# Kernel tuning notes

Hardware: AMD Instinct MI355X
Metric: run time of the kernel (lower is better)

The kernel has to match this reference:

```python
import jax, jax.numpy as jnp
import numpy as np

EMB = 512        # embedding_size (asserted == 512 in ColorClassifier)
NPC = 256        # n_possible_colors (asserted == 256)


def setup_inputs() -> dict:
    key = jax.random.key(0)
    ks = jax.random.split(key, 8)
    N, D = 8192, 16
    s = 0.05  # small init scale keeps softmax/log numerically sane
    adj = jax.random.randint(ks[0], (N, D), 0, N, dtype=jnp.int32)
    W = jax.random.normal(ks[1], (EMB + NPC, EMB), jnp.float32) * s
    a = jax.random.normal(ks[2], (2 * EMB,), jnp.float32) * s
    fc1_w = jax.random.normal(ks[3], (EMB, EMB), jnp.float32) * s
    fc1_b = jnp.zeros((EMB,), jnp.float32)
    fc2_w = jax.random.normal(ks[4], (400, EMB), jnp.float32) * s
    fc2_b = jnp.zeros((400,), jnp.float32)
    fc3_w = jax.random.normal(ks[5], (NPC + 1, 400), jnp.float32) * s
    fc3_b = jnp.zeros((NPC + 1,), jnp.float32)
    return dict(adj=adj, W=W, a=a, fc1_w=fc1_w, fc1_b=fc1_b,
                fc2_w=fc2_w, fc2_b=fc2_b, fc3_w=fc3_w, fc3_b=fc3_b,
                baseline=50)


def _forward(adj, W, a, fc1_w, fc1_b, fc2_w, fc2_b, fc3_w, fc3_b, baseline):
    N, D = adj.shape
    alpha = 0.2           # GAT leaky-relu slope
    a1, a2 = a[:EMB], a[EMB:]
    NEG = -jnp.inf

    emb0 = jnp.zeros((N, EMB), jnp.float32)
    oh0 = jnp.zeros((N, NPC), jnp.float32).at[0, 0].set(1.0)   # vertex 0 gets color 0
    colors0 = jnp.full((N,), -1, jnp.int32).at[0].set(0)
    idx = jnp.arange(NPC + 1)

    def step(carry, v):
        emb, oh, colors, n_used, lpp = carry
        nbrs = adj[v]  # [D]
        # --- GAT singular attention update of vertex v (self row first) ---
        x = jnp.concatenate([
            jnp.concatenate([emb[v][None], emb[nbrs]], axis=0),
            jnp.concatenate([oh[v][None], oh[nbrs]], axis=0)], axis=1)  # [D+1, 768]
        h = x @ W                                           # [D+1, 512]
        e = jax.nn.leaky_relu(h[0] @ a1 + h @ a2, alpha)    # [D+1]
        attn = jax.nn.softmax(e)
        new_e = jax.nn.elu(attn @ h)                        # [512]
        emb = emb.at[v].set(new_e)
        # --- ColorClassifier MLP (leaky_relu slope 0.01 = torch default) ---
        h1 = jax.nn.leaky_relu(new_e @ fc1_w.T + fc1_b, 0.01)
        h2 = jax.nn.leaky_relu(h1 @ fc2_w.T + fc2_b, 0.01)
        logits = h2 @ fc3_w.T + fc3_b                       # [257]
        # mask unused colors [n_used, 256) (the 'new color' slot 256 stays open)
        irrel = (idx >= n_used) & (idx < NPC)
        # mask colors already used by neighbors (unassigned = -1 dropped)
        nc = colors[nbrs]
        safe = jnp.where(nc >= 0, nc, NPC + 1)              # out-of-range -> dropped
        adj_mask = jnp.zeros((NPC + 1,), bool).at[safe].set(True, mode='drop')
        probs = jax.nn.softmax(jnp.where(irrel | adj_mask, NEG, logits))
        max_idx = jnp.argmax(probs).astype(jnp.int32)
        is_new = (max_idx == NPC)
        chosen = jnp.where(is_new, n_used, max_idx)
        n_used = n_used + is_new.astype(jnp.int32)
        colors = colors.at[v].set(chosen)
        oh = oh.at[v].set(jax.nn.one_hot(chosen, NPC, dtype=jnp.float32))
        lpp = lpp + jnp.log(jnp.max(probs) + 1e-8) - jnp.log(jnp.float32(1e-8))
        return (emb, oh, colors, n_used, lpp), None

    carry0 = (emb0, oh0, colors0, jnp.int32(1), jnp.float32(0.0))
    (emb, oh, colors, n_used, lpp), _ = jax.lax.scan(step, carry0, jnp.arange(1, N))

    reg = (jnp.linalg.norm(W) + jnp.linalg.norm(fc1_w)
           + jnp.linalg.norm(fc2_w) + jnp.linalg.norm(fc3_w))
    loss = (n_used.astype(jnp.float32) - jnp.float32(baseline)) * lpp / N + 0.05 * reg
    return colors, loss


def reference(adj, W, a, fc1_w, fc1_b, fc2_w, fc2_b, fc3_w, fc3_b, baseline):
    return _forward(adj, W, a, fc1_w, fc1_b, fc2_w, fc2_b, fc3_w, fc3_b, baseline)
```

## Files before the change

### kernel.cpp

```cpp
#include <hip/hip_runtime.h>
#include <math.h>

#define NV    8192
#define DEG   16
#define EMBD  512
#define NPCC  256
#define NL    257
#define GBLK  32
#define TPB   512
#define K     12

#define WS_FLAG  0
#define WS_SSQ   4096
#define WS_OHD   5120
#define WS_H1    8192
#define WS_H2    57344
#define WS_LOG   106496
#define WS_NWE   131456
#define WS_EHP   180608
#define WS_EHV   188800
#define WS_HF    221568

struct __align__(16) Smem {
  float wembT[16*512];
  float fc1[16*512];
  float fc2[13*512];
  float fc3[9*512];
  float ohdot[256];
  float a2[512];
  float newe8[K][512];
  float e[K][20];
  float attn[K][20];
  float hev[K][16];
  float bpv[K];
  int   biv[K];
  float fc1b[16];
  float fc2b[16];
  float fc3b[16];
  float red[32];
  float scalf[4];
  int   scali[4];
  int   nbrs[8][K][16];
  int   bmeta[8][2];
  int   chosen[K];
  int   slotbad[K];
  unsigned char colors[NV];
};
static_assert(sizeof(Smem) <= 160*1024, "LDS overflow");

__device__ __forceinline__ float dot4(const float4 a, const float4 b) {
  return a.x*b.x + a.y*b.y + a.z*b.z + a.w*b.w;
}
__device__ __forceinline__ float red64_add(float x) {
  #pragma unroll
  for (int off = 1; off < 64; off <<= 1) x += __shfl_xor(x, off, 64);
  return x;
}
__device__ __forceinline__ float red16_add(float x) {
  #pragma unroll
  for (int off = 1; off < 16; off <<= 1) x += __shfl_xor(x, off, 64);
  return x;
}

__device__ __forceinline__ void d_scan(const unsigned char* colors, const int* nbrsD,
                                       const float* lg, int nused, int lane,
                                       float& bp_out, int& bi_out) {
  int nc[DEG];
  #pragma unroll
  for (int j = 0; j < DEG; ++j) nc[j] = (int)colors[nbrsD[j]] - 1;
  float sv[5]; float bmx = -INFINITY;
  #pragma unroll
  for (int p = 0; p < 5; ++p) {
    int idx = lane + p*64;
    float val = -INFINITY;
    if (idx < NL) {
      val = lg[idx];
      bool msk = (idx >= nused) && (idx < NPCC);
      #pragma unroll
      for (int j = 0; j < DEG; ++j) msk |= (idx == nc[j]);
      if (msk) val = -INFINITY;
    }
    sv[p] = val;
    bmx = fmaxf(bmx, val);
  }
  #pragma unroll
  for (int off = 1; off < 64; off <<= 1) bmx = fmaxf(bmx, __shfl_xor(bmx, off, 64));
  float ssum = 0.f;
  #pragma unroll
  for (int p = 0; p < 5; ++p) ssum += expf(sv[p] - bmx);
  #pragma unroll
  for (int off = 1; off < 64; off <<= 1) ssum += __shfl_xor(ssum, off, 64);
  float bp = -1.f; int bi = NL + 10;
  #pragma unroll
  for (int p = 0; p < 5; ++p) {
    int idx = lane + p*64;
    float pj = (idx < NL) ? (expf(sv[p] - bmx) / ssum) : -1.f;
    if (pj > bp) { bp = pj; bi = idx; }
  }
  #pragma unroll
  for (int off = 1; off < 64; off <<= 1) {
    float op = __shfl_xor(bp, off, 64);
    int   oi = __shfl_xor(bi, off, 64);
    if (op > bp || (op == bp && oi < bi)) { bp = op; bi = oi; }
  }
  bp_out = bp; bi_out = bi;
}

__global__ void __launch_bounds__(TPB, 1)
gc_kernel(const int* __restrict__ adj, const float* __restrict__ W,
          const float* __restrict__ a, const float* __restrict__ fc1w,
          const float* __restrict__ fc1b_g, const float* __restrict__ fc2w,
          const float* __restrict__ fc2b_g, const float* __restrict__ fc3w,
          const float* __restrict__ fc3b_g, const int* __restrict__ basep,
          float* __restrict__ out, unsigned char* __restrict__ ws)
{
  extern __shared__ char smem_raw[];
  Smem& S = *reinterpret_cast<Smem*>(smem_raw);
  const int b    = blockIdx.x;
  const int t    = threadIdx.x;
  const int wave = t >> 6;
  const int lane = t & 63;
  const int g    = lane >> 4;
  const int j16  = lane & 15;

  unsigned* flags = (unsigned*)(ws + WS_FLAG);
  float* ssqP  = (float*)(ws + WS_SSQ);
  float* ohdg  = (float*)(ws + WS_OHD);
  float* h1g   = (float*)(ws + WS_H1);
  float* h2g   = (float*)(ws + WS_H2);
  float* logg  = (float*)(ws + WS_LOG);
  float* nweg  = (float*)(ws + WS_NWE);
  float* eHpg  = (float*)(ws + WS_EHP);
  float* eHvg  = (float*)(ws + WS_EHV);
  float* HF    = (float*)(ws + WS_HF);

  const int kbase  = b * 16;
  const int nrows2 = (b < 16) ? 13 : 12;
  const int base2  = (b < 16) ? 13*b : 208 + 12*(b-16);
  const int nrows3 = (b == 0) ? 9 : 8;
  const int base3  = (b == 0) ? 0 : 8*b + 1;

  for (int i = t; i < EMBD; i += TPB) S.a2[i] = a[EMBD + i];
  for (int i = t; i < 16*512; i += TPB) S.fc1[i] = fc1w[(size_t)kbase*512 + i];
  for (int i = t; i < 13*512; i += TPB) {
    int rr = i >> 9;
    S.fc2[i] = (rr < nrows2) ? fc2w[(size_t)base2*512 + i] : 0.f;
  }
  for (int i = t; i < 9*512; i += TPB) {
    int rr = i >> 9, cc = i & 511;
    S.fc3[i] = (rr < nrows3 && cc < 400) ? fc3w[(size_t)(base3+rr)*400 + cc] : 0.f;
  }
  for (int i = t; i < 512; i += TPB) {
    const float* src = W + (size_t)i*512 + kbase;
    #pragma unroll
    for (int kk = 0; kk < 16; ++kk) S.wembT[kk*512 + i] = src[kk];
  }
  if (t < 16) {
    S.fc1b[t] = fc1b_g[kbase + t];
    S.fc2b[t] = (t < nrows2) ? fc2b_g[base2 + t] : 0.f;
    S.fc3b[t] = (t < nrows3) ? fc3b_g[base3 + t] : 0.f;
  }
  for (int i = t; i < NV/4; i += TPB) ((int*)S.colors)[i] = 0;
  if (t < 16) ((int*)S.bmeta)[t] = 0;
  if (t == 0) {
    S.colors[0] = 1;
    S.scali[0] = 1;
    S.scalf[0] = 0.f;
  }
  {
    int c = b*8 + wave;
    const float* wr = W + (size_t)(512 + c)*512;
    float acc = 0.f;
    #pragma unroll
    for (int p = 0; p < 2; ++p) {
      float4 w4 = *(const float4*)&wr[p*256 + lane*4];
      float4 a4 = *(const float4*)&a[EMBD + p*256 + lane*4];
      acc += dot4(w4, a4);
    }
    acc = red64_add(acc);
    if (lane == 0) {
      ohdg[c] = acc;
      if (c == 0) eHvg[0] = acc;
    }
  }
  __syncthreads();
  if (t < 16) HF[kbase + t] = W[(size_t)512*512 + kbase + t];
  {
    float s0=0.f, s1=0.f, s2=0.f, s3=0.f;
    for (int i = t; i < 16*512; i += TPB) {
      float x = S.wembT[i]; s0 += x*x;
      x = S.fc1[i]; s1 += x*x;
    }
    for (int i = t; i < 13*512; i += TPB) { float x = S.fc2[i]; s2 += x*x; }
    for (int i = t; i < 9*512; i += TPB)  { float x = S.fc3[i]; s3 += x*x; }
    for (int i = t; i < 4096; i += TPB) {
      int c = i >> 4, kk = i & 15;
      float x = W[(size_t)(512 + c)*512 + kbase + kk];
      s0 += x*x;
    }
    s0 = red64_add(s0); s1 = red64_add(s1); s2 = red64_add(s2); s3 = red64_add(s3);
    if (lane == 0) { S.red[wave*4+0]=s0; S.red[wave*4+1]=s1; S.red[wave*4+2]=s2; S.red[wave*4+3]=s3; }
    __syncthreads();
    if (t == 0) {
      for (int m = 0; m < 4; ++m) {
        float s = 0.f;
        for (int w = 0; w < 8; ++w) s += S.red[w*4 + m];
        ssqP[m*GBLK + b] = s;
      }
    }
  }
  unsigned ep = 1;
  __syncthreads();
  if (t == 0) __hip_atomic_store(&flags[b*32], ep, __ATOMIC_RELEASE, __HIP_MEMORY_SCOPE_AGENT);
  if (t < 32) {
    while (__hip_atomic_load(&flags[t*32], __ATOMIC_RELAXED, __HIP_MEMORY_SCOPE_AGENT) < ep) { }
  }
  if (t == 0) (void)__hip_atomic_load(&flags[0], __ATOMIC_ACQUIRE, __HIP_MEMORY_SCOPE_AGENT);
  __syncthreads();

  if (t < 256) S.ohdot[t] = ohdg[t];
  if (b == 0 && t == 0) {
    float reg = 0.f;
    for (int m = 0; m < 4; ++m) {
      float s = 0.f;
      for (int bb = 0; bb < GBLK; ++bb) s += ssqP[m*GBLK + bb];
      reg += sqrtf(s);
    }
    S.scalf[1] = reg;
  }
  __syncthreads();

  int va = 1, d_done = 0;
  unsigned T = 0;

  #pragma unroll 1
  for (;;) {
    const int tk   = (int)(T & 7);
    const int iA2  = (int)((T+7) & 7);
    const int iB   = (int)((T+6) & 7);
    const int iC   = (int)((T+5) & 7);
    const int iD   = (int)((T+4) & 7);
    const int v0A2 = S.bmeta[iA2][0], nA2 = S.bmeta[iA2][1];
    const int nB   = S.bmeta[iB][1];
    const int nC   = S.bmeta[iC][1];
    const int v0D  = S.bmeta[iD][0],  nD  = S.bmeta[iD][1];
    const bool canA = (va < NV);
    const int Kc = canA ? ((NV - va < K) ? (NV - va) : K) : 0;
    const int pT  = (int)(T & 1);
    const int pT1 = pT ^ 1;
    const float* lgD = logg + pT*(K*260);

    if (t < Kc*DEG) {
      int s = t >> 4, j = t & 15;
      int v = va + s;
      int u = adj[v*DEG + j];
      S.nbrs[tk][s][j] = u;
      bool bad = false;
      float er = 0.f;
      if (u < v) {
        if (u > d_done) bad = true;
        else { float eh = eHvg[u]; er = (eh >= 0.f) ? eh : 0.2f*eh; }
      }
      S.e[s][j+1] = er;
      unsigned long long bm = __ballot(bad);
      if (j == 0) S.slotbad[s] = (int)((bm >> (((t >> 4) & 3)*16)) & 0xFFFFull);
    }
    if (t < K) S.e[t][0] = 0.f;
    for (int x = t; x < nA2*128; x += TPB)
      ((float4*)S.newe8)[x] = ((const float4*)(nweg + pT1*(K*512)))[x];
    const int grp = t >> 4;
    const int tot = nB + nC;
    float4 xr[8];
    const bool hasJob = (grp < tot);
    const bool isB = hasJob && (grp < nB);
    const int s2j = isB ? grp : grp - nB;
    if (hasJob) {
      const float* xp = isB ? (h1g + pT*(K*512) + s2j*512)
                            : (h2g + pT1*(K*512) + s2j*512);
      #pragma unroll
      for (int tt = 0; tt < 8; ++tt) xr[tt] = *(const float4*)&xp[j16*4 + tt*64];
    }
    __syncthreads();

    int n = 0;
    while (n < Kc && S.slotbad[n] == 0) ++n;
    if (t == 0) { S.bmeta[tk][0] = va; S.bmeta[tk][1] = n; }

    if (wave == 2 && lane < n) {
      float m = 0.f;
      #pragma unroll
      for (int j = 1; j <= DEG; ++j) m = fmaxf(m, S.e[lane][j]);
      float ex[DEG+1]; float ssum = 0.f;
      #pragma unroll
      for (int j = 0; j <= DEG; ++j) { ex[j] = expf(S.e[lane][j] - m); ssum += ex[j]; }
      #pragma unroll
      for (int j = 0; j <= DEG; ++j) S.attn[lane][j] = ex[j] / ssum;
    }
    float ppre[K];
    #pragma unroll
    for (int s2 = 0; s2 < K; ++s2) ppre[s2] = 0.f;
    if (b == 0 && wave == 0 && lane < 32) {
      #pragma unroll
      for (int s2 = 0; s2 < K; ++s2)
        if (s2 < nD) ppre[s2] = eHpg[((v0D+s2)&63)*32 + lane];
    }
    {
      const int nspec = S.scali[0];
      #pragma unroll
      for (int rep = 0; rep < 2; ++rep) {
        int s2 = wave + rep*8;
        if (s2 < nD) {
          float bp; int bi;
          d_scan(S.colors, S.nbrs[iD][s2], lgD + s2*260, nspec, lane, bp, bi);
          if (lane == 0) { S.bpv[s2] = bp; S.biv[s2] = bi; }
        }
      }
    }
    if (hasJob) {
      const int nr = isB ? nrows2 : nrows3;
      const float* wbase = isB ? S.fc2 : S.fc3;
      const float* bb    = isB ? S.fc2b : S.fc3b;
      for (int r = 0; r < 13; ++r) {
        if (r >= nr) break;
        float acc = 0.f;
        const float* wrow = wbase + r*512;
        #pragma unroll
        for (int tt = 0; tt < 8; ++tt) {
          float4 w4 = *(const float4*)&wrow[j16*4 + tt*64];
          acc += dot4(xr[tt], w4);
        }
        acc = red16_add(acc);
        if (j16 == 0) {
          if (isB) {
            float hvv = acc + bb[r];
            h2g[pT*(K*512) + s2j*512 + base2 + r] = (hvv >= 0.f) ? hvv : 0.01f*hvv;
          } else {
            logg[pT1*(K*260) + s2j*260 + base3 + r] = acc + bb[r];
          }
        }
      }
    }
    {
      const int r = (wave & 3)*4 + g;
      const bool doFc1 = (wave < 4);
      const float* wrow = doFc1 ? (S.fc1 + r*512) : (S.wembT + r*512);
      float acc[K];
      #pragma unroll
      for (int s = 0; s < K; ++s) acc[s] = 0.f;
      #pragma unroll
      for (int tt = 0; tt < 8; ++tt) {
        float4 w4 = *(const float4*)&wrow[j16*4 + tt*64];
        #pragma unroll
        for (int s = 0; s < K; ++s) {
          if (s < nA2) {
            float4 x4 = *(const float4*)&S.newe8[s][j16*4 + tt*64];
            acc[s] += dot4(x4, w4);
          }
        }
      }
      #pragma unroll
      for (int s = 0; s < K; ++s) {
        if (s < nA2) {
          float ar = red16_add(acc[s]);
          if (j16 == 0) {
            if (doFc1) {
              float hvv = ar + S.fc1b[r];
              h1g[pT1*(K*512) + s*512 + kbase + r] = (hvv >= 0.f) ? hvv : 0.01f*hvv;
            } else {
              HF[(size_t)(v0A2+s)*EMBD + kbase + r] = ar;
              S.hev[s][r] = ar;
            }
          }
        }
      }
    }
    __syncthreads();

    if (wave == 0) {
      if (nD > 0) {
        int nused = S.scali[0];
        const int nspec = nused;
        float lpp = S.scalf[0];
        #pragma unroll 1
        for (int s2 = 0; s2 < nD; ++s2) {
          const int vD = v0D + s2;
          float bp; int bi;
          if (nused == nspec) { bp = S.bpv[s2]; bi = S.biv[s2]; }
          else {
            d_scan(S.colors, S.nbrs[iD][s2], lgD + s2*260, nused, lane, bp, bi);
          }
          const int isnew  = (bi == NPCC) ? 1 : 0;
          const int chosen = isnew ? nused : bi;
          nused += isnew;
          lpp += logf(bp + 1e-8f) - logf(1e-8f);
          if (lane == 0) {
            S.colors[vD] = (unsigned char)(chosen + 1);
            S.chosen[s2] = chosen;
          }
          if (b == 0) {
            float pp = (lane < 32) ? ppre[s2] : 0.f;
            #pragma unroll
            for (int off = 1; off < 32; off <<= 1) pp += __shfl_xor(pp, off, 64);
            if (lane == 0) eHvg[vD] = pp + S.ohdot[chosen];
          }
        }
        if (lane == 0) { S.scali[0] = nused; S.scalf[0] = lpp; }
      }
    } else {
      const int s = (t - 64) >> 4;
      const int c = t & 15;
      if (s < n) {
        const int vv = va + s;
        float gv[16];
        #pragma unroll
        for (int j = 0; j < 16; ++j) {
          int u = S.nbrs[tk][s][j];
          gv[j] = (u < vv) ? HF[(size_t)u*EMBD + kbase + c] : 0.f;
        }
        float acc = 0.f;
        #pragma unroll
        for (int j = 0; j < 16; ++j) acc += S.attn[s][j+1] * gv[j];
        float nv = (acc > 0.f) ? acc : expm1f(acc);
        nweg[pT*(K*512) + s*512 + kbase + c] = nv;
      }
    }
    __syncthreads();

    if (t < nD*16) {
      const int fsp = t >> 4, fj = t & 15;
      HF[(size_t)(v0D+fsp)*EMBD + kbase + fj] +=
          W[(size_t)(512 + S.chosen[fsp])*512 + kbase + fj];
    }
    if (t < nA2) {
      float pp = 0.f;
      #pragma unroll
      for (int kk = 0; kk < 16; ++kk) pp += S.hev[t][kk] * S.a2[kbase + kk];
      eHpg[((v0A2+t)&63)*32 + b] = pp;
    }
    __syncthreads();
    ++ep;
    if (t == 0) __hip_atomic_store(&flags[b*32], ep, __ATOMIC_RELEASE, __HIP_MEMORY_SCOPE_AGENT);
    if (t < 32) {
      while (__hip_atomic_load(&flags[t*32], __ATOMIC_RELAXED, __HIP_MEMORY_SCOPE_AGENT) < ep) { }
    }
    if (t == 0) (void)__hip_atomic_load(&flags[0], __ATOMIC_ACQUIRE, __HIP_MEMORY_SCOPE_AGENT);
    __syncthreads();

    if (nD > 0) d_done = v0D + nD - 1;
    va += n;
    ++T;
    if (d_done == NV-1) break;
    if (T > 12000u) break;
  }

  if (b == 0) {
    for (int i = t; i < NV; i += TPB) out[i] = (float)((int)S.colors[i] - 1);
    if (t == 0) {
      int bv = basep[0];
      int bl = (bv >= -100000 && bv <= 100000) ? bv : (int)__int_as_float(bv);
      float loss = ((float)(S.scali[0] - bl)) * S.scalf[0] / 8192.0f + 0.05f * S.scalf[1];
      out[NV] = loss;
    }
  }
}

extern "C" void kernel_launch(void* const* d_in, const int* in_sizes, int n_in,
                              void* d_out, int out_size, void* d_ws, size_t ws_size,
                              hipStream_t stream) {
  const int*   adj  = (const int*)d_in[0];
  const float* W    = (const float*)d_in[1];
  const float* av   = (const float*)d_in[2];
  const float* f1w  = (const float*)d_in[3];
  const float* f1b  = (const float*)d_in[4];
  const float* f2w  = (const float*)d_in[5];
  const float* f2b  = (const float*)d_in[6];
  const float* f3w  = (const float*)d_in[7];
  const float* f3b  = (const float*)d_in[8];
  const int*   bas  = (const int*)d_in[9];
  float* out = (float*)d_out;
  unsigned char* ws = (unsigned char*)d_ws;

  (void)hipMemsetAsync(d_ws, 0, 8192, stream);
  (void)hipFuncSetAttribute((const void*)gc_kernel,
                      hipFuncAttributeMaxDynamicSharedMemorySize,
                      (int)sizeof(Smem));
  gc_kernel<<<dim3(GBLK), dim3(TPB), sizeof(Smem), stream>>>(
      adj, W, av, f1w, f1b, f2w, f2b, f3w, f3b, bas, out, ws);
}
```

Before: 24.99 ms.

## Defer HF color update, prefetch logits, drop a barrier, widen batch K

Moves the HF one-hot row update into the next iteration, ahead of the first barrier, and folds the eHp partial dot into an idle thread group. Together these remove one __syncthreads per pipeline step. The logits for the D-stage scan are now loaded into registers before the barrier, so their global-load latency overlaps other work. Batch width K rises from 12 to 14 and the workspace offsets are resized to match, giving fewer grid-synchronised steps at the cost of more registers and LDS.

Result: no change. 24.61 ms (-1.5%).

```diff
diff --git a/kernel.cpp b/kernel.cpp
--- a/kernel.cpp
+++ b/kernel.cpp
@@ -8,18 +8,18 @@
 #define NL    257
 #define GBLK  32
 #define TPB   512
-#define K     12
+#define K     14
 
 #define WS_FLAG  0
 #define WS_SSQ   4096
 #define WS_OHD   5120
 #define WS_H1    8192
-#define WS_H2    57344
-#define WS_LOG   106496
-#define WS_NWE   131456
-#define WS_EHP   180608
-#define WS_EHV   188800
-#define WS_HF    221568
+#define WS_H2    65536
+#define WS_LOG   122880
+#define WS_NWE   152064
+#define WS_EHP   209408
+#define WS_EHV   217600
+#define WS_HF    262144
 
 struct __align__(16) Smem {
   float wembT[16*512];
@@ -62,9 +62,9 @@
   return x;
 }
 
-__device__ __forceinline__ void d_scan(const unsigned char* colors, const int* nbrsD,
-                                       const float* lg, int nused, int lane,
-                                       float& bp_out, int& bi_out) {
+__device__ __forceinline__ void d_scan_pre(const unsigned char* colors, const int* nbrsD,
+                                           const float svin[5], int nused, int lane,
+                                           float& bp_out, int& bi_out) {
   int nc[DEG];
   #pragma unroll
   for (int j = 0; j < DEG; ++j) nc[j] = (int)colors[nbrsD[j]] - 1;
@@ -72,14 +72,11 @@
   #pragma unroll
   for (int p = 0; p < 5; ++p) {
     int idx = lane + p*64;
-    float val = -INFINITY;
-    if (idx < NL) {
-      val = lg[idx];
-      bool msk = (idx >= nused) && (idx < NPCC);
-      #pragma unroll
-      for (int j = 0; j < DEG; ++j) msk |= (idx == nc[j]);
-      if (msk) val = -INFINITY;
-    }
+    float val = svin[p];
+    bool msk = (idx >= nused) && (idx < NPCC);
+    #pragma unroll
+    for (int j = 0; j < DEG; ++j) msk |= (idx == nc[j]);
+    if (msk || idx >= NL) val = -INFINITY;
     sv[p] = val;
     bmx = fmaxf(bmx, val);
   }
@@ -240,16 +237,23 @@
     const int iB   = (int)((T+6) & 7);
     const int iC   = (int)((T+5) & 7);
     const int iD   = (int)((T+4) & 7);
+    const int iF   = (int)((T+3) & 7);
     const int v0A2 = S.bmeta[iA2][0], nA2 = S.bmeta[iA2][1];
     const int nB   = S.bmeta[iB][1];
     const int nC   = S.bmeta[iC][1];
     const int v0D  = S.bmeta[iD][0],  nD  = S.bmeta[iD][1];
+    const int v0F  = S.bmeta[iF][0],  nF  = S.bmeta[iF][1];
     const bool canA = (va < NV);
     const int Kc = canA ? ((NV - va < K) ? (NV - va) : K) : 0;
     const int pT  = (int)(T & 1);
     const int pT1 = pT ^ 1;
     const float* lgD = logg + pT*(K*260);
 
+    if (t < nF*16) {
+      const int fsp = t >> 4, fj = t & 15;
+      HF[(size_t)(v0F+fsp)*EMBD + kbase + fj] +=
+          W[(size_t)(512 + S.chosen[fsp])*512 + kbase + fj];
+    }
     if (t < Kc*DEG) {
       int s = t >> 4, j = t & 15;
       int v = va + s;
@@ -280,21 +284,15 @@
       #pragma unroll
       for (int tt = 0; tt < 8; ++tt) xr[tt] = *(const float4*)&xp[j16*4 + tt*64];
     }
-    __syncthreads();
-
-    int n = 0;
-    while (n < Kc && S.slotbad[n] == 0) ++n;
-    if (t == 0) { S.bmeta[tk][0] = va; S.bmeta[tk][1] = n; }
-
-    if (wave == 2 && lane < n) {
-      float m = 0.f;
-      #pragma unroll
-      for (int j = 1; j <= DEG; ++j) m = fmaxf(m, S.e[lane][j]);
-      float ex[DEG+1]; float ssum = 0.f;
-      #pragma unroll
-      for (int j = 0; j <= DEG; ++j) { ex[j] = expf(S.e[lane][j] - m); ssum += ex[j]; }
-      #pragma unroll
-      for (int j = 0; j <= DEG; ++j) S.attn[lane][j] = ex[j] / ssum;
+    float svp[2][5];
+    #pragma unroll
+    for (int rep = 0; rep < 2; ++rep) {
+      int s2 = wave + rep*8;
+      #pragma unroll
+      for (int p = 0; p < 5; ++p) {
+        int idx = lane + p*64;
+        svp[rep][p] = (s2 < nD && idx < NL) ? lgD[s2*260 + idx] : -INFINITY;
+      }
     }
     float ppre[K];
     #pragma unroll
@@ -304,6 +302,22 @@
       for (int s2 = 0; s2 < K; ++s2)
         if (s2 < nD) ppre[s2] = eHpg[((v0D+s2)&63)*32 + lane];
     }
+    __syncthreads();
+
+    int n = 0;
+    while (n < Kc && S.slotbad[n] == 0) ++n;
+    if (t == 0) { S.bmeta[tk][0] = va; S.bmeta[tk][1] = n; }
+
+    if (wave == 2 && lane < n) {
+      float m = 0.f;
+      #pragma unroll
+      for (int j = 1; j <= DEG; ++j) m = fmaxf(m, S.e[lane][j]);
+      float ex[DEG+1]; float ssum = 0.f;
+      #pragma unroll
+      for (int j = 0; j <= DEG; ++j) { ex[j] = expf(S.e[lane][j] - m); ssum += ex[j]; }
+      #pragma unroll
+      for (int j = 0; j <= DEG; ++j) S.attn[lane][j] = ex[j] / ssum;
+    }
     {
       const int nspec = S.scali[0];
       #pragma unroll
@@ -311,7 +325,7 @@
         int s2 = wave + rep*8;
         if (s2 < nD) {
           float bp; int bi;
-          d_scan(S.colors, S.nbrs[iD][s2], lgD + s2*260, nspec, lane, bp, bi);
+          d_scan_pre(S.colors, S.nbrs[iD][s2], svp[rep], nspec, lane, bp, bi);
           if (lane == 0) { S.bpv[s2] = bp; S.biv[s2] = bi; }
         }
       }
@@ -387,7 +401,13 @@
           float bp; int bi;
           if (nused == nspec) { bp = S.bpv[s2]; bi = S.biv[s2]; }
           else {
-            d_scan(S.colors, S.nbrs[iD][s2], lgD + s2*260, nused, lane, bp, bi);
+            float sv[5];
+            #pragma unroll
+            for (int p = 0; p < 5; ++p) {
+              int idx = lane + p*64;
+              sv[p] = (idx < NL) ? lgD[s2*260 + idx] : -INFINITY;
+            }
+            d_scan_pre(S.colors, S.nbrs[iD][s2], sv, nused, lane, bp, bi);
           }
           const int isnew  = (bi == NPCC) ? 1 : 0;
           const int chosen = isnew ? nused : bi;
@@ -407,9 +427,10 @@
         if (lane == 0) { S.scali[0] = nused; S.scalf[0] = lpp; }
       }
     } else {
-      const int s = (t - 64) >> 4;
-      const int c = t & 15;
-      if (s < n) {
+      const int gi = (t - 64) >> 4;
+      if (gi < n) {
+        const int s = gi;
+        const int c = t & 15;
         const int vv = va + s;
         float gv[16];
         #pragma unroll
@@ -422,20 +443,15 @@
         for (int j = 0; j < 16; ++j) acc += S.attn[s][j+1] * gv[j];
         float nv = (acc > 0.f) ? acc : expm1f(acc);
         nweg[pT*(K*512) + s*512 + kbase + c] = nv;
-      }
-    }
-    __syncthreads();
-
-    if (t < nD*16) {
-      const int fsp = t >> 4, fj = t & 15;
-      HF[(size_t)(v0D+fsp)*EMBD + kbase + fj] +=
-          W[(size_t)(512 + S.chosen[fsp])*512 + kbase + fj];
-    }
-    if (t < nA2) {
-      float pp = 0.f;
-      #pragma unroll
-      for (int kk = 0; kk < 16; ++kk) pp += S.hev[t][kk] * S.a2[kbase + kk];
-      eHpg[((v0A2+t)&63)*32 + b] = pp;
+      } else if (gi == 27) {
+        const int s = t & 15;
+        if (s < nA2) {
+          float pp = 0.f;
+          #pragma unroll
+          for (int kk = 0; kk < 16; ++kk) pp += S.hev[s][kk] * S.a2[kbase + kk];
+          eHpg[((v0A2+s)&63)*32 + b] = pp;
+        }
+      }
     }
     __syncthreads();
     ++ep;
```
